# Kernel optimization log

Hardware: AMD Instinct MI355X
Metric: run time of the kernel (lower is better)

Reference implementation:

```python
import jax, jax.numpy as jnp
import numpy as np

B, SEQ, D, N_LAYERS, HEADS, D_FF = 256, 43, 18, 6, 3, 2048
A_MAX, NB = 128, 7
EPS = 1e-6


def _norm(x, a, b):
    mu = x.mean(-1, keepdims=True)
    sd = jnp.std(x, axis=-1, ddof=1, keepdims=True)  # torch std is unbiased
    return a * (x - mu) / (sd + EPS) + b


def _attn(x, Wq, bq, Wk, bk, Wv, bv, Wo, bo, mask):
    b_, s, d = x.shape
    dk = d // HEADS
    def split_heads(W, bb):
        return (x @ W + bb).reshape(b_, s, HEADS, dk).transpose(0, 2, 1, 3)
    q, k, v = split_heads(Wq, bq), split_heads(Wk, bk), split_heads(Wv, bv)
    scores = jnp.einsum('bhqd,bhkd->bhqk', q, k) / jnp.sqrt(jnp.float32(dk))
    scores = jnp.where(mask[:, None, :, :] == 0, -1e9, scores)  # mask [B,1,S] -> [B,1,1,S]
    attn = jax.nn.softmax(scores, axis=-1)
    o = jnp.einsum('bhqk,bhkd->bhqd', attn, v).transpose(0, 2, 1, 3).reshape(b_, s, d)
    return o @ Wo + bo


def setup_inputs() -> dict:
    key = jax.random.key(0)
    ks = iter(jax.random.split(key, 40))
    g = lambda shape, s=0.05: jax.random.normal(next(ks), shape, dtype=jnp.float32) * s
    inp = {
        'src': jax.random.normal(next(ks), (B, SEQ, D), dtype=jnp.float32),
        'mask': jnp.ones((B, 1, SEQ), dtype=jnp.int32),
        'max_atoms': A_MAX,
        'enc_Wq': g((N_LAYERS, D, D)), 'enc_bq': g((N_LAYERS, D)),
        'enc_Wk': g((N_LAYERS, D, D)), 'enc_bk': g((N_LAYERS, D)),
        'enc_Wv': g((N_LAYERS, D, D)), 'enc_bv': g((N_LAYERS, D)),
        'enc_Wo': g((N_LAYERS, D, D)), 'enc_bo': g((N_LAYERS, D)),
        'enc_ln1_a': jnp.ones((N_LAYERS, D), jnp.float32), 'enc_ln1_b': jnp.zeros((N_LAYERS, D), jnp.float32),
        'enc_ln2_a': jnp.ones((N_LAYERS, D), jnp.float32), 'enc_ln2_b': jnp.zeros((N_LAYERS, D), jnp.float32),
        'enc_ffW1': g((N_LAYERS, D, D_FF)), 'enc_ffb1': g((N_LAYERS, D_FF)),
        'enc_ffW2': g((N_LAYERS, D_FF, D)), 'enc_ffb2': g((N_LAYERS, D)),
        'll2_W': g((D, A_MAX)), 'll2_b': g((A_MAX,)),
        'll_W': g((SEQ, A_MAX)), 'll_b': g((A_MAX,)),
        'fl_W': g((2 * A_MAX, NB)), 'fl_b': g((NB,)),
    }
    return inp


def reference(src, enc_Wq, enc_bq, enc_Wk, enc_bk, enc_Wv, enc_bv, enc_Wo, enc_bo,
              enc_ln1_a, enc_ln1_b, enc_ln2_a, enc_ln2_b,
              enc_ffW1, enc_ffb1, enc_ffW2, enc_ffb2,
              ll2_W, ll2_b, ll_W, ll_b, fl_W, fl_b, mask, max_atoms):
    # --- Encoder (dropout=0 at eval; no final norm, as in source) ---
    x = src
    for i in range(N_LAYERS):
        x2 = _norm(x, enc_ln1_a[i], enc_ln1_b[i])
        x = x + _attn(x2, enc_Wq[i], enc_bq[i], enc_Wk[i], enc_bk[i],
                      enc_Wv[i], enc_bv[i], enc_Wo[i], enc_bo[i], mask)
        x2 = _norm(x, enc_ln2_a[i], enc_ln2_b[i])
        x = x + (jax.nn.relu(x2 @ enc_ffW1[i] + enc_ffb1[i]) @ enc_ffW2[i] + enc_ffb2[i])
    # --- EdgeClassify2 ---
    red = x @ ll2_W + ll2_b            # [B, S, A]
    red = red.transpose(0, 2, 1)       # [B, A, S]
    R = red @ ll_W + ll_b              # [B, A, A]; repeat_e[:,i,i,:] == R[:,i,:]
    # final_e[b,i,j] = concat(R[b,i], R[b,j]); fl(concat) = R_i@W1 + R_j@W2 + b (exact)
    W1, W2 = fl_W[:max_atoms], fl_W[max_atoms:]
    P = R @ W1                          # [B, A, nb]
    Q = R @ W2                          # [B, A, nb]
    return P[:, :, None, :] + Q[:, None, :, :] + fl_b  # [B, A, A, nb]
```

## Files before the change

### kernel.cpp

```cpp
#include <hip/hip_runtime.h>
#include <math.h>

namespace {

constexpr int Sq = 43;
constexpr int Dm = 18;
constexpr int Dff = 2048;
constexpr int Am = 128;
constexpr int Nb = 7;
constexpr int NR = 11008;
constexpr int RSZ = NR * Dm;
constexpr int JC = 8;
constexpr int WROW = 20;
constexpr float EPSf = 1e-6f;

__global__ __launch_bounds__(64) void k_attn(
    int layer,
    const float* __restrict__ Xi, float* __restrict__ Xn,
    float* __restrict__ x2g, const float* __restrict__ Pp,
    const int* __restrict__ maskg,
    const float* __restrict__ Wq, const float* __restrict__ bq,
    const float* __restrict__ Wk, const float* __restrict__ bk,
    const float* __restrict__ Wv, const float* __restrict__ bv,
    const float* __restrict__ ln1a, const float* __restrict__ ln1b,
    const float* __restrict__ Wo, const float* __restrict__ bo,
    const float* __restrict__ ln2a, const float* __restrict__ ln2b,
    const float* __restrict__ b2g,
    const float* __restrict__ fW1g, const float* __restrict__ fb1g,
    const float* __restrict__ fW2g,
    float* __restrict__ W1P, float* __restrict__ W2P,
    const float* __restrict__ llW, const float* __restrict__ llb,
    const float* __restrict__ flW, const float* __restrict__ flb,
    const float* __restrict__ ll2b,
    float* __restrict__ Mw, float* __restrict__ PS1, float* __restrict__ QS2)
{
    __shared__ __align__(16) float ks[Sq * 20];
    __shared__ __align__(16) float vs[Sq * 20];
    __shared__ int ms[Sq];
    __shared__ float M[602];
    __shared__ float cc2[14];
    __shared__ float SS[14];

    const int tid = threadIdx.x;
    const int b = blockIdx.x;

    if (b >= 256) {
        if (b < 448) {
            const int idx = (b - 256) * 64 + tid;
            const int l = idx / Dff;
            const int j = idx - l * Dff;
            float* o1 = W1P + (size_t)idx * WROW;
            float* o2 = W2P + (size_t)idx * WROW;
            #pragma unroll
            for (int d = 0; d < Dm; d++)
                o1[d] = fW1g[(size_t)l * Dm * Dff + (size_t)d * Dff + j];
            o1[18] = fb1g[l * Dff + j];
            o1[19] = 0.f;
            #pragma unroll
            for (int d = 0; d < Dm; d++)
                o2[d] = fW2g[((size_t)l * Dff + j) * Dm + d];
            o2[18] = 0.f;
            o2[19] = 0.f;
            if (idx < WROW) {
                W1P[(size_t)6 * Dff * WROW + idx] = 0.f;
                W2P[(size_t)6 * Dff * WROW + idx] = 0.f;
            }
            return;
        }
        for (int m = tid; m < 602; m += 64) {
            int half = m / 301, rem = m - half * 301;
            int s = rem / 7, n = rem - 7 * s;
            float a = 0.f;
            for (int jj = 0; jj < Am; jj++)
                a += llW[s * Am + jj] * flW[(half * Am + jj) * Nb + n];
            M[m] = a;
        }
        if (tid < 14) {
            int half = tid / 7, n = tid - 7 * (tid / 7);
            float a = 0.f;
            for (int jj = 0; jj < Am; jj++)
                a += llb[jj] * flW[(half * Am + jj) * Nb + n];
            cc2[tid] = a;
        }
        __syncthreads();
        if (tid < 14) {
            int half = tid / 7, n = tid - 7 * (tid / 7);
            float s2 = 0.f;
            for (int s = 0; s < Sq; s++) s2 += M[half * 301 + s * 7 + n];
            SS[tid] = s2;
        }
        __syncthreads();
        for (int m = tid; m < 602; m += 64) Mw[m] = M[m];
        for (int m = tid; m < 896; m += 64) {
            int i = m / 7, n = m - 7 * i;
            PS1[m] = cc2[n] + ll2b[i] * SS[n];
            QS2[m] = cc2[7 + n] + ll2b[i] * SS[7 + n] + flb[n];
        }
        return;
    }

    const float scale = 0.40824829046386296f;

    if (tid < Sq) ms[tid] = maskg[b * Sq + tid];

    float y[Dm];
    float qv[Dm];
    if (tid < Sq) {
        const size_t ro = (size_t)(b * Sq + tid) * Dm;
        #pragma unroll
        for (int d = 0; d < Dm; d++) {
            float t = Xi[ro + d];
            if (layer > 0) {
                #pragma unroll
                for (int c = 0; c < JC; c++) t += Pp[(size_t)c * RSZ + ro + d];
            }
            y[d] = t;
        }
        float mu = 0.f;
        #pragma unroll
        for (int d = 0; d < Dm; d++) mu += y[d];
        mu *= (1.f / Dm);
        float var = 0.f;
        #pragma unroll
        for (int d = 0; d < Dm; d++) { float t = y[d] - mu; var += t * t; }
        var *= (1.f / (Dm - 1));
        float isd = 1.f / (sqrtf(var) + EPSf);
        float x2[Dm];
        #pragma unroll
        for (int d = 0; d < Dm; d++)
            x2[d] = ln1a[layer * Dm + d] * (y[d] - mu) * isd
                  + ln1b[layer * Dm + d];
        const float* wqp = Wq + layer * Dm * Dm;
        const float* wkp = Wk + layer * Dm * Dm;
        const float* wvp = Wv + layer * Dm * Dm;
        #pragma unroll 3
        for (int d = 0; d < Dm; d++) {
            float aq = bq[layer * Dm + d];
            float ak = bk[layer * Dm + d];
            float av = bv[layer * Dm + d];
            #pragma unroll
            for (int dd = 0; dd < Dm; dd++) {
                aq += x2[dd] * wqp[dd * Dm + d];
                ak += x2[dd] * wkp[dd * Dm + d];
                av += x2[dd] * wvp[dd * Dm + d];
            }
            qv[d] = aq;
            ks[tid * 20 + d] = ak;
            vs[tid * 20 + d] = av;
        }
    }
    __syncthreads();
    if (tid >= Sq) return;

    float o[Dm];
    #pragma unroll
    for (int h = 0; h < 3; h++) {
        float sum = 0.f;
        float o6[6];
        #pragma unroll
        for (int d = 0; d < 6; d++) o6[d] = 0.f;
        const float q0 = qv[h * 6], q1 = qv[h * 6 + 1], q2 = qv[h * 6 + 2];
        const float q3 = qv[h * 6 + 3], q4 = qv[h * 6 + 4], q5 = qv[h * 6 + 5];
        for (int j = 0; j < Sq; j++) {
            const float* kr = ks + j * 20 + h * 6;
            const float2 k0 = *(const float2*)(kr);
            const float2 k1 = *(const float2*)(kr + 2);
            const float2 k2 = *(const float2*)(kr + 4);
            float t = q0 * k0.x + q1 * k0.y + q2 * k1.x +
                      q3 * k1.y + q4 * k2.x + q5 * k2.y;
            t *= scale;
            if (ms[j] == 0) t = -1e9f;
            float e = __expf(t);
            sum += e;
            const float* vr = vs + j * 20 + h * 6;
            const float2 v0 = *(const float2*)(vr);
            const float2 v1 = *(const float2*)(vr + 2);
            const float2 v2 = *(const float2*)(vr + 4);
            o6[0] += e * v0.x; o6[1] += e * v0.y; o6[2] += e * v1.x;
            o6[3] += e * v1.y; o6[4] += e * v2.x; o6[5] += e * v2.y;
        }
        float inv = 1.f / sum;
        #pragma unroll
        for (int d = 0; d < 6; d++) o[h * 6 + d] = o6[d] * inv;
    }

    const float* wo = Wo + layer * Dm * Dm;
    float yo[Dm];
    #pragma unroll 3
    for (int d = 0; d < Dm; d++) {
        float t = bo[layer * Dm + d];
        #pragma unroll
        for (int dd = 0; dd < Dm; dd++) t += o[dd] * wo[dd * Dm + d];
        yo[d] = y[d] + t;
    }
    const size_t ro = (size_t)(b * Sq + tid) * Dm;
    #pragma unroll
    for (int d = 0; d < Dm; d++)
        Xn[ro + d] = yo[d] + b2g[layer * Dm + d];
    float mu = 0.f;
    #pragma unroll
    for (int d = 0; d < Dm; d++) mu += yo[d];
    mu *= (1.f / Dm);
    float var = 0.f;
    #pragma unroll
    for (int d = 0; d < Dm; d++) { float t = yo[d] - mu; var += t * t; }
    var *= (1.f / (Dm - 1));
    float isd = 1.f / (sqrtf(var) + EPSf);
    #pragma unroll
    for (int d = 0; d < Dm; d++)
        x2g[ro + d] =
            ln2a[layer * Dm + d] * (yo[d] - mu) * isd + ln2b[layer * Dm + d];
}

__global__ __launch_bounds__(256, 3) void k_ffn(
    int layer, const float* __restrict__ x2g,
    const float* __restrict__ W1P, const float* __restrict__ W2P,
    float* __restrict__ P)
{
    __shared__ float Ls[4 * 64 * Dm];

    const int tid  = threadIdx.x;
    const int lane = tid & 63;
    const int wv   = __builtin_amdgcn_readfirstlane(tid >> 6);
    const int rg   = blockIdx.x >> 3;
    const int q    = blockIdx.x & 7;
    const int row  = rg * 64 + lane;
    const int j0   = q * 256 + wv * 64;

    const float4* w1p = (const float4*)(W1P + ((size_t)layer * Dff + j0) * WROW);
    const float4* w2p = (const float4*)(W2P + ((size_t)layer * Dff + j0) * WROW);

    float x[Dm];
    #pragma unroll
    for (int k = 0; k < 9; k++) {
        float2 t = *(const float2*)(x2g + (size_t)row * Dm + 2 * k);
        x[2 * k] = t.x; x[2 * k + 1] = t.y;
    }
    float acc[Dm];
    #pragma unroll
    for (int d = 0; d < Dm; d++) acc[d] = 0.f;

    float4 a0 = w1p[0], a1 = w1p[1], a2 = w1p[2], a3 = w1p[3], a4 = w1p[4];
    float4 c0 = w2p[0], c1 = w2p[1], c2 = w2p[2], c3 = w2p[3], c4 = w2p[4];

    for (int jj = 0; jj < 64; jj++) {
        const float4* n1 = w1p + (jj + 1) * 5;
        const float4* n2 = w2p + (jj + 1) * 5;
        const float4 na0 = n1[0], na1 = n1[1], na2 = n1[2], na3 = n1[3], na4 = n1[4];
        const float4 nc0 = n2[0], nc1 = n2[1], nc2 = n2[2], nc3 = n2[3], nc4 = n2[4];

        float h = a4.z
            + x[0]  * a0.x + x[1]  * a0.y + x[2]  * a0.z + x[3]  * a0.w
            + x[4]  * a1.x + x[5]  * a1.y + x[6]  * a1.z + x[7]  * a1.w
            + x[8]  * a2.x + x[9]  * a2.y + x[10] * a2.z + x[11] * a2.w
            + x[12] * a3.x + x[13] * a3.y + x[14] * a3.z + x[15] * a3.w
            + x[16] * a4.x + x[17] * a4.y;
        h = fmaxf(h, 0.f);
        acc[0]  += h * c0.x;  acc[1]  += h * c0.y;
        acc[2]  += h * c0.z;  acc[3]  += h * c0.w;
        acc[4]  += h * c1.x;  acc[5]  += h * c1.y;
        acc[6]  += h * c1.z;  acc[7]  += h * c1.w;
        acc[8]  += h * c2.x;  acc[9]  += h * c2.y;
        acc[10] += h * c2.z;  acc[11] += h * c2.w;
        acc[12] += h * c3.x;  acc[13] += h * c3.y;
        acc[14] += h * c3.z;  acc[15] += h * c3.w;
        acc[16] += h * c4.x;  acc[17] += h * c4.y;

        a0 = na0; a1 = na1; a2 = na2; a3 = na3; a4 = na4;
        c0 = nc0; c1 = nc1; c2 = nc2; c3 = nc3; c4 = nc4;
    }

    #pragma unroll
    for (int d = 0; d < Dm; d++)
        Ls[(wv * 64 + lane) * Dm + d] = acc[d];
    __syncthreads();
    for (int e = tid; e < 1152; e += 256) {
        float s = Ls[e] + Ls[1152 + e] + Ls[2304 + e] + Ls[3456 + e];
        P[(size_t)q * RSZ + (size_t)rg * 1152 + e] = s;
    }
}

__global__ __launch_bounds__(256) void k_out(
    const float* __restrict__ xg, const float* __restrict__ Pp,
    const float* __restrict__ ll2W,
    const float* __restrict__ Mw, const float* __restrict__ PS1,
    const float* __restrict__ QS2, float* __restrict__ out)
{
    __shared__ float xb[Sq * Dm];
    __shared__ float M[602];
    __shared__ float T[2][Dm][Nb];
    __shared__ float Pc[32 * Nb];
    __shared__ float QBs[Am * Nb];

    const int b = blockIdx.y, chunk = blockIdx.x, tid = threadIdx.x;

    for (int e = tid; e < Sq * Dm; e += 256) {
        const size_t o = (size_t)b * (Sq * Dm) + e;
        float t = xg[o];
        #pragma unroll
        for (int c = 0; c < JC; c++) t += Pp[(size_t)c * RSZ + o];
        xb[e] = t;
    }
    for (int m = tid; m < 602; m += 256) M[m] = Mw[m];
    __syncthreads();

    for (int m = tid; m < 252; m += 256) {
        int half = m / 126, rem = m - half * 126;
        int d = rem / 7, n = rem - 7 * d;
        float a = 0.f;
        for (int s = 0; s < Sq; s++)
            a += xb[s * Dm + d] * M[half * 301 + s * 7 + n];
        T[half][d][n] = a;
    }
    __syncthreads();

    for (int m = tid; m < 224; m += 256) {
        int il = m / 7, n = m - 7 * il;
        int i = chunk * 32 + il;
        float a = PS1[i * 7 + n];
        #pragma unroll
        for (int d = 0; d < Dm; d++) a += T[0][d][n] * ll2W[d * Am + i];
        Pc[m] = a;
    }
    for (int e = tid; e < 896; e += 256) {
        int jj = e / 7, n = e - 7 * jj;
        float a = QS2[e];
        #pragma unroll
        for (int d = 0; d < Dm; d++) a += T[1][d][n] * ll2W[d * Am + jj];
        QBs[e] = a;
    }
    __syncthreads();

    if (tid < 224) {
        const int e = 4 * tid;
        const float q0 = QBs[e], q1 = QBs[e + 1], q2 = QBs[e + 2], q3 = QBs[e + 3];
        const int n0 = e % 7, n1 = (e + 1) % 7, n2 = (e + 2) % 7, n3 = (e + 3) % 7;
        const size_t base = (size_t)b * (Am * Am * Nb)
                          + (size_t)chunk * 32 * 896 + e;
        for (int il = 0; il < 32; il++) {
            const float* pc = Pc + il * 7;
            float4 v;
            v.x = pc[n0] + q0; v.y = pc[n1] + q1;
            v.z = pc[n2] + q2; v.w = pc[n3] + q3;
            *(float4*)(out + base + (size_t)il * 896) = v;
        }
    }
}

}

extern "C" void kernel_launch(void* const* d_in, const int* in_sizes, int n_in,
                              void* d_out, int out_size, void* d_ws, size_t ws_size,
                              hipStream_t stream)
{
    (void)in_sizes; (void)n_in; (void)out_size; (void)ws_size;

    const float* src  = (const float*)d_in[0];
    const int*   mask = (const int*)  d_in[1];
    const float* Wq   = (const float*)d_in[3];
    const float* bq   = (const float*)d_in[4];
    const float* Wk   = (const float*)d_in[5];
    const float* bk   = (const float*)d_in[6];
    const float* Wv   = (const float*)d_in[7];
    const float* bv   = (const float*)d_in[8];
    const float* Wo   = (const float*)d_in[9];
    const float* bo   = (const float*)d_in[10];
    const float* ln1a = (const float*)d_in[11];
    const float* ln1b = (const float*)d_in[12];
    const float* ln2a = (const float*)d_in[13];
    const float* ln2b = (const float*)d_in[14];
    const float* fW1  = (const float*)d_in[15];
    const float* fb1  = (const float*)d_in[16];
    const float* fW2  = (const float*)d_in[17];
    const float* fb2  = (const float*)d_in[18];
    const float* ll2W = (const float*)d_in[19];
    const float* ll2b = (const float*)d_in[20];
    const float* llW  = (const float*)d_in[21];
    const float* llb  = (const float*)d_in[22];
    const float* flW  = (const float*)d_in[23];
    const float* flb  = (const float*)d_in[24];
    float* out = (float*)d_out;

    const size_t WPSZ = (size_t)6 * Dff * WROW + WROW;

    float* ws  = (float*)d_ws;
    float* xA  = ws;
    float* xB  = ws + 1 * (size_t)RSZ;
    float* x2g = ws + 2 * (size_t)RSZ;
    float* P   = ws + 3 * (size_t)RSZ;
    float* W1P = ws + (3 + JC) * (size_t)RSZ;
    float* W2P = W1P + WPSZ;
    float* Mw  = W2P + WPSZ;
    float* PS1 = Mw + 604;
    float* QS2 = PS1 + 896;

    for (int i = 0; i < 6; i++) {
        const float* Xi = (i == 0) ? src : ((i % 2 == 1) ? xB : xA);
        float*       Xn = (i % 2 == 0) ? xB : xA;
        const int nblk = (i == 0) ? 449 : 256;
        k_attn<<<nblk, 64, 0, stream>>>(i, Xi, Xn, x2g, P, mask,
                                        Wq, bq, Wk, bk, Wv, bv,
                                        ln1a, ln1b, Wo, bo, ln2a, ln2b, fb2,
                                        fW1, fb1, fW2, W1P, W2P,
                                        llW, llb, flW, flb, ll2b,
                                        Mw, PS1, QS2);
        k_ffn<<<1376, 256, 0, stream>>>(i, x2g, W1P, W2P, P);
    }
    k_out<<<dim3(4, 256), 256, 0, stream>>>(xA, P, ll2W, Mw, PS1, QS2, out);
}
```

Before: 568.9 us.

## Accumulate FFN partial sums into residual with atomics instead of partial buffers

```diff
diff --git a/kernel.cpp b/kernel.cpp
--- a/kernel.cpp
+++ b/kernel.cpp
@@ -10,14 +10,13 @@
 constexpr int Nb = 7;
 constexpr int NR = 11008;
 constexpr int RSZ = NR * Dm;
-constexpr int JC = 8;
 constexpr int WROW = 20;
 constexpr float EPSf = 1e-6f;
 
 __global__ __launch_bounds__(64) void k_attn(
     int layer,
     const float* __restrict__ Xi, float* __restrict__ Xn,
-    float* __restrict__ x2g, const float* __restrict__ Pp,
+    float* __restrict__ x2g,
     const int* __restrict__ maskg,
     const float* __restrict__ Wq, const float* __restrict__ bq,
     const float* __restrict__ Wk, const float* __restrict__ bk,
@@ -108,13 +107,9 @@
     if (tid < Sq) {
         const size_t ro = (size_t)(b * Sq + tid) * Dm;
         #pragma unroll
-        for (int d = 0; d < Dm; d++) {
-            float t = Xi[ro + d];
-            if (layer > 0) {
-                #pragma unroll
-                for (int c = 0; c < JC; c++) t += Pp[(size_t)c * RSZ + ro + d];
-            }
-            y[d] = t;
+        for (int k = 0; k < 9; k++) {
+            float2 t = *(const float2*)(Xi + ro + 2 * k);
+            y[2 * k] = t.x; y[2 * k + 1] = t.y;
         }
         float mu = 0.f;
         #pragma unroll
@@ -215,7 +210,7 @@
 __global__ __launch_bounds__(256, 3) void k_ffn(
     int layer, const float* __restrict__ x2g,
     const float* __restrict__ W1P, const float* __restrict__ W2P,
-    float* __restrict__ P)
+    float* __restrict__ Xn)
 {
     __shared__ float Ls[4 * 64 * Dm];
 
@@ -276,12 +271,12 @@
     __syncthreads();
     for (int e = tid; e < 1152; e += 256) {
         float s = Ls[e] + Ls[1152 + e] + Ls[2304 + e] + Ls[3456 + e];
-        P[(size_t)q * RSZ + (size_t)rg * 1152 + e] = s;
+        unsafeAtomicAdd(&Xn[(size_t)rg * 1152 + e], s);
     }
 }
 
 __global__ __launch_bounds__(256) void k_out(
-    const float* __restrict__ xg, const float* __restrict__ Pp,
+    const float* __restrict__ xg,
     const float* __restrict__ ll2W,
     const float* __restrict__ Mw, const float* __restrict__ PS1,
     const float* __restrict__ QS2, float* __restrict__ out)
@@ -294,13 +289,8 @@
 
     const int b = blockIdx.y, chunk = blockIdx.x, tid = threadIdx.x;
 
-    for (int e = tid; e < Sq * Dm; e += 256) {
-        const size_t o = (size_t)b * (Sq * Dm) + e;
-        float t = xg[o];
-        #pragma unroll
-        for (int c = 0; c < JC; c++) t += Pp[(size_t)c * RSZ + o];
-        xb[e] = t;
-    }
+    for (int e = tid; e < Sq * Dm; e += 256)
+        xb[e] = xg[(size_t)b * (Sq * Dm) + e];
     for (int m = tid; m < 602; m += 256) M[m] = Mw[m];
     __syncthreads();
 
@@ -387,8 +377,7 @@
     float* xA  = ws;
     float* xB  = ws + 1 * (size_t)RSZ;
     float* x2g = ws + 2 * (size_t)RSZ;
-    float* P   = ws + 3 * (size_t)RSZ;
-    float* W1P = ws + (3 + JC) * (size_t)RSZ;
+    float* W1P = ws + 3 * (size_t)RSZ;
     float* W2P = W1P + WPSZ;
     float* Mw  = W2P + WPSZ;
     float* PS1 = Mw + 604;
@@ -398,13 +387,13 @@
         const float* Xi = (i == 0) ? src : ((i % 2 == 1) ? xB : xA);
         float*       Xn = (i % 2 == 0) ? xB : xA;
         const int nblk = (i == 0) ? 449 : 256;
-        k_attn<<<nblk, 64, 0, stream>>>(i, Xi, Xn, x2g, P, mask,
+        k_attn<<<nblk, 64, 0, stream>>>(i, Xi, Xn, x2g, mask,
                                         Wq, bq, Wk, bk, Wv, bv,
                                         ln1a, ln1b, Wo, bo, ln2a, ln2b, fb2,
                                         fW1, fb1, fW2, W1P, W2P,
                                         llW, llb, flW, flb, ll2b,
                                         Mw, PS1, QS2);
-        k_ffn<<<1376, 256, 0, stream>>>(i, x2g, W1P, W2P, P);
-    }
-    k_out<<<dim3(4, 256), 256, 0, stream>>>(xA, P, ll2W, Mw, PS1, QS2, out);
-}
+        k_ffn<<<1376, 256, 0, stream>>>(i, x2g, W1P, W2P, Xn);
+    }
+    k_out<<<dim3(4, 256), 256, 0, stream>>>(xA, ll2W, Mw, PS1, QS2, out);
+}
```

After: 537.7 us. 5.5% less time.
